# Kernel tuning notes

Hardware: AMD Instinct MI355X
Metric: run time of the kernel (lower is better)

The kernel has to match this reference:

```python
import jax, jax.numpy as jnp
import numpy as np

# GraphConvolutionSparse forward:
#   x = sparse_dropout(X)            (dropout=0.0 -> identity, kept faithful)
#   h = X @ W                        (sparse-dense matmul via segment_sum)
#   h = A @ h                        (sparse-dense matmul via segment_sum)
#   out = relu(h)

DROPOUT = 0.0  # layer default; keep_prob = 1 - dropout

def setup_inputs() -> dict:
    key = jax.random.key(0)
    k1, k2, k3, k4, k5, k6, k7 = jax.random.split(key, 7)
    N = 100000       # nodes
    D_IN = 512       # input feature dim
    D_OUT = 128      # output feature dim
    NNZ_X = 800000   # nonzeros in sparse feature matrix
    N_E = 1600000    # adjacency nonzeros (edges)
    x_vals = jax.random.normal(k1, (NNZ_X,), dtype=jnp.float32)
    x_rows = jax.random.randint(k2, (NNZ_X,), 0, N, dtype=jnp.int32)
    x_cols = jax.random.randint(k3, (NNZ_X,), 0, D_IN, dtype=jnp.int32)
    adj_vals = jax.random.uniform(k4, (N_E,), dtype=jnp.float32)
    adj_rows = jax.random.randint(k5, (N_E,), 0, N, dtype=jnp.int32)
    adj_cols = jax.random.randint(k6, (N_E,), 0, N, dtype=jnp.int32)
    init_range = np.sqrt(6.0 / (D_IN + D_OUT)).astype(np.float32)
    W = jax.random.uniform(k7, (D_IN, D_OUT), minval=-init_range, maxval=init_range, dtype=jnp.float32)
    return {"x_vals": x_vals, "x_rows": x_rows, "x_cols": x_cols,
            "adj_vals": adj_vals, "adj_rows": adj_rows, "adj_cols": adj_cols,
            "W": W, "n_nodes": N}

def reference(x_vals, x_rows, x_cols, adj_vals, adj_rows, adj_cols, W, n_nodes):
    keep_prob = 1.0 - DROPOUT
    # sparse dropout: with dropout=0.0 the mask keeps all entries and scale is 1,
    # so it reduces to the deterministic identity (faithful to tf semantics).
    vals = x_vals * (1.0 / keep_prob)
    # h = X @ W : gather weight rows by feature column, scale, scatter-add by node row
    xw = jax.ops.segment_sum(vals[:, None] * W[x_cols], x_rows, num_segments=n_nodes)  # [N, D_OUT]
    # out = A @ h : gather source-node rows, scale by edge weight, scatter-add to dest
    agg = jax.ops.segment_sum(adj_vals[:, None] * xw[adj_cols], adj_rows, num_segments=n_nodes)  # [N, D_OUT]
    return jax.nn.relu(agg)
```

## Files before the change

kernel.cpp:

```cpp
#include <hip/hip_runtime.h>
#include <hip/hip_fp16.h>


#define DOUT 128
#define RB 64
#define RB_BITS 6
#define NBMAX 2048
#define CAPL 2048
#define COLMASK 131071
#define CTH 256
#define CWAVES 4
#define CAPX 768
#define CAPA 1408

static inline size_t align_up(size_t x, size_t a) { return (x + a - 1) & ~(a - 1); }

__device__ inline int wave_incl_scan(int v, int lane) {
    #pragma unroll
    for (int off = 1; off < 64; off <<= 1) {
        int up = __shfl_up(v, off, 64);
        if (lane >= off) v += up;
    }
    return v;
}

__global__ __launch_bounds__(256) void wh_precompute(const float* __restrict__ W,
                                                     __half2* __restrict__ Wh, int total) {
    int i = blockIdx.x * 256 + threadIdx.x;
    if (i < total) {
        int c = i >> 6, l = i & 63;
        Wh[i] = __floats2half2_rn(W[(c << 7) + 2 * l], W[(c << 7) + 2 * l + 1]);
    }
}

__global__ __launch_bounds__(256) void hist_coarse(const int* __restrict__ xr, int nx,
                                                   const int* __restrict__ ar, int na,
                                                   int* __restrict__ cx, int* __restrict__ ca) {
    __shared__ int h[2 * NBMAX];
    for (int i = threadIdx.x; i < 2 * NBMAX; i += 256) h[i] = 0;
    __syncthreads();
    int base = blockIdx.x * 4096;
    int tot = nx + na;
    #pragma unroll
    for (int k = 0; k < 16; ++k) {
        int i = base + k * 256 + threadIdx.x;
        if (i < tot) {
            if (i < nx) atomicAdd(&h[xr[i] >> RB_BITS], 1);
            else        atomicAdd(&h[NBMAX + (ar[i - nx] >> RB_BITS)], 1);
        }
    }
    __syncthreads();
    for (int i = threadIdx.x; i < 2 * NBMAX; i += 256) {
        int c = h[i];
        if (c) {
            if (i < NBMAX) atomicAdd(&cx[i], c);
            else           atomicAdd(&ca[i - NBMAX], c);
        }
    }
}

__global__ __launch_bounds__(1024) void scan_nb(const int* __restrict__ cx, const int* __restrict__ ca,
                                                int* __restrict__ bx, int* __restrict__ ba,
                                                int* __restrict__ curx, int* __restrict__ cura, int nb) {
    const int* c = blockIdx.x ? ca : cx;
    int* bs  = blockIdx.x ? ba : bx;
    int* cur = blockIdx.x ? cura : curx;
    __shared__ int wsum[16];
    __shared__ int woff[16];
    __shared__ int carry_s, chunk_tot;
    int tid = threadIdx.x, lane = tid & 63, wid = tid >> 6;
    if (tid == 0) carry_s = 0;
    __syncthreads();
    for (int base = 0; base < nb; base += 1024) {
        int i = base + tid;
        int v = (i < nb) ? c[i] : 0;
        int incl = wave_incl_scan(v, lane);
        if (lane == 63) wsum[wid] = incl;
        __syncthreads();
        if (wid == 0 && lane < 16) {
            int s = wsum[lane];
            int is = s;
            #pragma unroll
            for (int off = 1; off < 16; off <<= 1) {
                int up = __shfl_up(is, off, 64);
                if (lane >= off) is += up;
            }
            woff[lane] = is - s;
            if (lane == 15) chunk_tot = is;
        }
        __syncthreads();
        int excl = incl - v + woff[wid] + carry_s;
        if (i < nb) { bs[i] = excl; cur[i] = excl; }
        __syncthreads();
        if (tid == 0) carry_s += chunk_tot;
        __syncthreads();
    }
    if (tid == 0) bs[nb] = carry_s;
}

__global__ __launch_bounds__(512) void bucket_scatter2(const int* __restrict__ xr, const int* __restrict__ xc,
                                                       const float* __restrict__ xv, int nx,
                                                       const int* __restrict__ ar, const int* __restrict__ ac,
                                                       const float* __restrict__ av, int na,
                                                       int* __restrict__ curx, int* __restrict__ cura,
                                                       int2* __restrict__ stx, int2* __restrict__ sta,
                                                       int nb, int nblk_x, int capx, int capa) {
    const int* rows; const int* cols; const float* vals; int n; int* gcur; int2* stage; int base; int cap;
    if (blockIdx.x < nblk_x) {
        rows = xr; cols = xc; vals = xv; n = nx; gcur = curx; stage = stx;
        base = blockIdx.x * 4096; cap = capx;
    } else {
        rows = ar; cols = ac; vals = av; n = na; gcur = cura; stage = sta;
        base = (blockIdx.x - nblk_x) * 4096; cap = capa;
    }
    __shared__ int h[NBMAX];
    __shared__ int bcur[NBMAX];
    for (int i = threadIdx.x; i < nb; i += 512) h[i] = 0;
    __syncthreads();
    int rr[8]; int cc[8]; float vv[8];
    #pragma unroll
    for (int k = 0; k < 8; ++k) {
        int i = base + k * 512 + threadIdx.x;
        rr[k] = -1;
        if (i < n) {
            rr[k] = rows[i]; cc[k] = cols[i]; vv[k] = vals[i];
            atomicAdd(&h[rr[k] >> RB_BITS], 1);
        }
    }
    __syncthreads();
    for (int b = threadIdx.x; b < nb; b += 512) {
        int c = h[b];
        if (c) {
            int r = atomicAdd(&gcur[b], c);
            bcur[b] = (cap > 0) ? (b * cap + r) : r;
        }
    }
    __syncthreads();
    #pragma unroll
    for (int k = 0; k < 8; ++k) {
        if (rr[k] >= 0) {
            int b = rr[k] >> RB_BITS;
            int p = atomicAdd(&bcur[b], 1);
            if (cap == 0 || p < b * cap + cap)
                stage[p] = make_int2(((rr[k] & (RB - 1)) << 17) | cc[k], __float_as_int(vv[k]));
        }
    }
}

__global__ __launch_bounds__(CTH) void consumer_xw(const int* __restrict__ bx, const int* __restrict__ gcnt,
                                                   const int2* __restrict__ stage,
                                                   const __half2* __restrict__ Wh, __half2* __restrict__ xwh,
                                                   int N, int cap) {
    __shared__ int2 sp[CAPL];
    __shared__ int hoff[RB + 1];
    __shared__ int curs[RB];
    int b = blockIdx.x;
    int s, cnt;
    if (cap > 0) { s = b * cap; cnt = min(gcnt[b], cap); }
    else         { s = bx[b]; cnt = bx[b + 1] - s; }
    int tid = threadIdx.x, lane = tid & 63, wid = tid >> 6;
    bool fast = (cnt <= CAPL);
    if (tid < RB) curs[tid] = 0;
    __syncthreads();
    if (fast) {
        for (int i = tid; i < cnt; i += CTH)
            atomicAdd(&curs[(stage[s + i].x >> 17) & (RB - 1)], 1);
    }
    __syncthreads();
    if (wid == 0) {
        int v = curs[lane];
        int incl = wave_incl_scan(v, lane);
        int excl = incl - v;
        hoff[lane] = excl;
        curs[lane] = excl;
        if (lane == 63) hoff[RB] = incl;
    }
    __syncthreads();
    if (fast) {
        for (int i = tid; i < cnt; i += CTH) {
            int2 p = stage[s + i];
            int r = (p.x >> 17) & (RB - 1);
            sp[atomicAdd(&curs[r], 1)] = p;
        }
    }
    __syncthreads();
    int row0 = b << RB_BITS;
    #pragma unroll 1
    for (int rr = 0; rr < RB / CWAVES; ++rr) {
        int r = wid + rr * CWAVES;
        int grow = row0 + r;
        if (grow >= N) continue;
        float ax = 0.f, ay = 0.f;
        if (fast) {
            int j = hoff[r], o1 = hoff[r + 1];
            for (; j + 3 < o1; j += 4) {
                int2 c0 = sp[j], c1 = sp[j + 1], c2 = sp[j + 2], c3 = sp[j + 3];
                float2 w0 = __half22float2(Wh[((size_t)(c0.x & COLMASK) << 6) + lane]);
                float2 w1 = __half22float2(Wh[((size_t)(c1.x & COLMASK) << 6) + lane]);
                float2 w2 = __half22float2(Wh[((size_t)(c2.x & COLMASK) << 6) + lane]);
                float2 w3 = __half22float2(Wh[((size_t)(c3.x & COLMASK) << 6) + lane]);
                float v0 = __int_as_float(c0.y), v1 = __int_as_float(c1.y);
                float v2 = __int_as_float(c2.y), v3 = __int_as_float(c3.y);
                ax += v0 * w0.x + v1 * w1.x + v2 * w2.x + v3 * w3.x;
                ay += v0 * w0.y + v1 * w1.y + v2 * w2.y + v3 * w3.y;
            }
            for (; j < o1; ++j) {
                int2 c0 = sp[j];
                float2 w0 = __half22float2(Wh[((size_t)(c0.x & COLMASK) << 6) + lane]);
                float v0 = __int_as_float(c0.y);
                ax += v0 * w0.x; ay += v0 * w0.y;
            }
        } else {
            for (int j = 0; j < cnt; ++j) {
                int2 c0 = stage[s + j];
                if (((c0.x >> 17) & (RB - 1)) == r) {
                    float2 w0 = __half22float2(Wh[((size_t)(c0.x & COLMASK) << 6) + lane]);
                    float v0 = __int_as_float(c0.y);
                    ax += v0 * w0.x; ay += v0 * w0.y;
                }
            }
        }
        xwh[((size_t)grow << 6) + lane] = __float22half2_rn(make_float2(ax, ay));
    }
}

__global__ __launch_bounds__(CTH) void consumer_adj(const int* __restrict__ ba, const int* __restrict__ gcnt,
                                                    const int2* __restrict__ stage,
                                                    const __half2* __restrict__ xwh, float* __restrict__ out,
                                                    int N, int cap) {
    __shared__ int2 sp[CAPL];
    __shared__ int hoff[RB + 1];
    __shared__ int curs[RB];
    int b = blockIdx.x;
    int s, cnt;
    if (cap > 0) { s = b * cap; cnt = min(gcnt[b], cap); }
    else         { s = ba[b]; cnt = ba[b + 1] - s; }
    int tid = threadIdx.x, lane = tid & 63, wid = tid >> 6;
    bool fast = (cnt <= CAPL);
    if (tid < RB) curs[tid] = 0;
    __syncthreads();
    if (fast) {
        for (int i = tid; i < cnt; i += CTH)
            atomicAdd(&curs[(stage[s + i].x >> 17) & (RB - 1)], 1);
    }
    __syncthreads();
    if (wid == 0) {
        int v = curs[lane];
        int incl = wave_incl_scan(v, lane);
        int excl = incl - v;
        hoff[lane] = excl;
        curs[lane] = excl;
        if (lane == 63) hoff[RB] = incl;
    }
    __syncthreads();
    if (fast) {
        for (int i = tid; i < cnt; i += CTH) {
            int2 p = stage[s + i];
            int r = (p.x >> 17) & (RB - 1);
            sp[atomicAdd(&curs[r], 1)] = p;
        }
    }
    __syncthreads();
    int row0 = b << RB_BITS;
    #pragma unroll 1
    for (int rr = 0; rr < RB / CWAVES; ++rr) {
        int r = wid + rr * CWAVES;
        int grow = row0 + r;
        if (grow >= N) continue;
        float ax = 0.f, ay = 0.f;
        if (fast) {
            int j = hoff[r], o1 = hoff[r + 1];
            for (; j + 3 < o1; j += 4) {
                int2 c0 = sp[j], c1 = sp[j + 1], c2 = sp[j + 2], c3 = sp[j + 3];
                float2 h0 = __half22float2(xwh[((size_t)(c0.x & COLMASK) << 6) + lane]);
                float2 h1 = __half22float2(xwh[((size_t)(c1.x & COLMASK) << 6) + lane]);
                float2 h2 = __half22float2(xwh[((size_t)(c2.x & COLMASK) << 6) + lane]);
                float2 h3 = __half22float2(xwh[((size_t)(c3.x & COLMASK) << 6) + lane]);
                float v0 = __int_as_float(c0.y), v1 = __int_as_float(c1.y);
                float v2 = __int_as_float(c2.y), v3 = __int_as_float(c3.y);
                ax += v0 * h0.x + v1 * h1.x + v2 * h2.x + v3 * h3.x;
                ay += v0 * h0.y + v1 * h1.y + v2 * h2.y + v3 * h3.y;
            }
            for (; j < o1; ++j) {
                int2 c0 = sp[j];
                float2 h0 = __half22float2(xwh[((size_t)(c0.x & COLMASK) << 6) + lane]);
                float v0 = __int_as_float(c0.y);
                ax += v0 * h0.x; ay += v0 * h0.y;
            }
        } else {
            for (int j = 0; j < cnt; ++j) {
                int2 c0 = stage[s + j];
                if (((c0.x >> 17) & (RB - 1)) == r) {
                    float2 h0 = __half22float2(xwh[((size_t)(c0.x & COLMASK) << 6) + lane]);
                    float v0 = __int_as_float(c0.y);
                    ax += v0 * h0.x; ay += v0 * h0.y;
                }
            }
        }
        ((float2*)(out + (size_t)grow * DOUT))[lane] = make_float2(fmaxf(ax, 0.f), fmaxf(ay, 0.f));
    }
}

__global__ void spmm_xw_atomic(const float* __restrict__ x_vals, const int* __restrict__ x_rows,
                               const int* __restrict__ x_cols, const float* __restrict__ W,
                               float* __restrict__ xw, int nnz) {
    long long t = (long long)blockIdx.x * blockDim.x + threadIdx.x;
    int i = (int)(t >> 7), d = (int)(t & 127);
    if (i >= nnz) return;
    atomicAdd(&xw[(long long)x_rows[i] * DOUT + d], x_vals[i] * W[(long long)x_cols[i] * DOUT + d]);
}
__global__ void spmm_adj_atomic(const float* __restrict__ adj_vals, const int* __restrict__ adj_rows,
                                const int* __restrict__ adj_cols, const float* __restrict__ xw,
                                float* __restrict__ out, int n_e) {
    long long t = (long long)blockIdx.x * blockDim.x + threadIdx.x;
    int e = (int)(t >> 7), d = (int)(t & 127);
    if (e >= n_e) return;
    atomicAdd(&out[(long long)adj_rows[e] * DOUT + d], adj_vals[e] * xw[(long long)adj_cols[e] * DOUT + d]);
}
__global__ void relu_kernel(float4* __restrict__ out, int n4) {
    int i = blockIdx.x * blockDim.x + threadIdx.x;
    if (i >= n4) return;
    float4 v = out[i];
    v.x = fmaxf(v.x, 0.f); v.y = fmaxf(v.y, 0.f);
    v.z = fmaxf(v.z, 0.f); v.w = fmaxf(v.w, 0.f);
    out[i] = v;
}

extern "C" void kernel_launch(void* const* d_in, const int* in_sizes, int n_in,
                              void* d_out, int out_size, void* d_ws, size_t ws_size,
                              hipStream_t stream) {
    const float* x_vals   = (const float*)d_in[0];
    const int*   x_rows   = (const int*)d_in[1];
    const int*   x_cols   = (const int*)d_in[2];
    const float* adj_vals = (const float*)d_in[3];
    const int*   adj_rows = (const int*)d_in[4];
    const int*   adj_cols = (const int*)d_in[5];
    const float* W        = (const float*)d_in[6];
    float* out = (float*)d_out;

    const int nnz_x = in_sizes[0];
    const int n_e   = in_sizes[3];
    const int N     = out_size / DOUT;
    const int D_IN  = in_sizes[6] / DOUT;
    const int nb    = (N + RB - 1) / RB;

    char* ws = (char*)d_ws;
    size_t off = 0;
    size_t xw_off   = off; off = align_up(off + (size_t)N * DOUT * sizeof(__half), 128);
    size_t wh_off   = off; off = align_up(off + (size_t)D_IN * 64 * sizeof(__half2), 128);
    size_t cx_off   = off; off += (size_t)NBMAX * sizeof(int);
    size_t ca_off   = off; off = align_up(off + (size_t)NBMAX * sizeof(int), 128);
    size_t bx_off   = off; off = align_up(off + (size_t)(NBMAX + 1) * sizeof(int), 128);
    size_t baoff    = off; off = align_up(off + (size_t)(NBMAX + 1) * sizeof(int), 128);
    size_t curx_off = off; off = align_up(off + (size_t)NBMAX * sizeof(int), 128);
    size_t cura_off = off; off = align_up(off + (size_t)NBMAX * sizeof(int), 128);
    size_t head = off;
    size_t sxc_off = head;
    size_t sac_off = align_up(sxc_off + (size_t)nb * CAPX * sizeof(int2), 128);
    size_t needed_cap = align_up(sac_off + (size_t)nb * CAPA * sizeof(int2), 128);
    size_t sxm_off = head;
    size_t sam_off = align_up(sxm_off + (size_t)nnz_x * sizeof(int2), 128);
    size_t needed_mid = align_up(sam_off + (size_t)n_e * sizeof(int2), 128);

    bool ok_dims = (nb <= NBMAX) && (N <= (COLMASK + 1));

    if (ok_dims && ws_size >= needed_cap) {
        __half2* xwh  = (__half2*)(ws + xw_off);
        __half2* Wh   = (__half2*)(ws + wh_off);
        int*  cx      = (int*)(ws + cx_off);
        int*  ca      = (int*)(ws + ca_off);
        int2* stage_x = (int2*)(ws + sxc_off);
        int2* stage_a = (int2*)(ws + sac_off);

        hipMemsetAsync(cx, 0, 2 * (size_t)NBMAX * sizeof(int), stream);
        int whtot = D_IN * 64;
        wh_precompute<<<(whtot + 255) / 256, 256, 0, stream>>>(W, Wh, whtot);

        int nblk_x = (nnz_x + 4095) / 4096;
        int nblk_a = (n_e + 4095) / 4096;
        bucket_scatter2<<<nblk_x + nblk_a, 512, 0, stream>>>(x_rows, x_cols, x_vals, nnz_x,
                                                             adj_rows, adj_cols, adj_vals, n_e,
                                                             cx, ca, stage_x, stage_a, nb, nblk_x,
                                                             CAPX, CAPA);
        consumer_xw<<<nb, CTH, 0, stream>>>(nullptr, cx, stage_x, Wh, xwh, N, CAPX);
        consumer_adj<<<nb, CTH, 0, stream>>>(nullptr, ca, stage_a, xwh, out, N, CAPA);
    } else if (ok_dims && ws_size >= needed_mid) {
        __half2* xwh  = (__half2*)(ws + xw_off);
        __half2* Wh   = (__half2*)(ws + wh_off);
        int*  cx      = (int*)(ws + cx_off);
        int*  ca      = (int*)(ws + ca_off);
        int*  bx      = (int*)(ws + bx_off);
        int*  ba      = (int*)(ws + baoff);
        int*  curx    = (int*)(ws + curx_off);
        int*  cura    = (int*)(ws + cura_off);
        int2* stage_x = (int2*)(ws + sxm_off);
        int2* stage_a = (int2*)(ws + sam_off);

        hipMemsetAsync(cx, 0, 2 * (size_t)NBMAX * sizeof(int), stream);
        int whtot = D_IN * 64;
        wh_precompute<<<(whtot + 255) / 256, 256, 0, stream>>>(W, Wh, whtot);

        int tot = nnz_x + n_e;
        hist_coarse<<<(tot + 4095) / 4096, 256, 0, stream>>>(x_rows, nnz_x, adj_rows, n_e, cx, ca);
        scan_nb<<<2, 1024, 0, stream>>>(cx, ca, bx, ba, curx, cura, nb);

        int nblk_x = (nnz_x + 4095) / 4096;
        int nblk_a = (n_e + 4095) / 4096;
        bucket_scatter2<<<nblk_x + nblk_a, 512, 0, stream>>>(x_rows, x_cols, x_vals, nnz_x,
                                                             adj_rows, adj_cols, adj_vals, n_e,
                                                             curx, cura, stage_x, stage_a, nb, nblk_x,
                                                             0, 0);
        consumer_xw<<<nb, CTH, 0, stream>>>(bx, nullptr, stage_x, Wh, xwh, N, 0);
        consumer_adj<<<nb, CTH, 0, stream>>>(ba, nullptr, stage_a, xwh, out, N, 0);
    } else {
        float* xw = (float*)ws;
        hipMemsetAsync(xw, 0, (size_t)out_size * sizeof(float), stream);
        hipMemsetAsync(out, 0, (size_t)out_size * sizeof(float), stream);
        long long t1 = (long long)nnz_x * DOUT;
        spmm_xw_atomic<<<(int)((t1 + 255) / 256), 256, 0, stream>>>(x_vals, x_rows, x_cols, W, xw, nnz_x);
        long long t2 = (long long)n_e * DOUT;
        spmm_adj_atomic<<<(int)((t2 + 255) / 256), 256, 0, stream>>>(adj_vals, adj_rows, adj_cols, xw, out, n_e);
        relu_kernel<<<(out_size / 4 + 255) / 256, 256, 0, stream>>>((float4*)out, out_size / 4);
    }
}
```

Before: 218.3 us.

## Use per-row counts from scatter and vectorized 16-lane-group gathers in consumers

The scatter kernel now also counts entries per row with global atomics, so both consumers can build row offsets directly instead of re-histogramming the staged entries in shared memory. The consumer inner loops are restructured so each group of 16 lanes handles one nonzero with 16-byte loads of a full 128-wide half row, four nonzeros per wave step, then reduces the partial sums across groups with shuffles. The separate memset is folded into a combined prep kernel that also converts W to half. This trades extra global atomics in the scatter for fewer shared-memory passes and wider, more parallel gathers. If a bucket overflows its capacity while the row total still fits the local buffer, the consumers can read uninitialised shared slots.

```diff
diff --git a/kernel.cpp b/kernel.cpp
--- a/kernel.cpp
+++ b/kernel.cpp
@@ -24,10 +24,12 @@
     return v;
 }
 
-__global__ __launch_bounds__(256) void wh_precompute(const float* __restrict__ W,
-                                                     __half2* __restrict__ Wh, int total) {
+__global__ __launch_bounds__(256) void prep_kernel(int* __restrict__ cnts, int ncnt,
+                                                   const float* __restrict__ W,
+                                                   __half2* __restrict__ Wh, int whtot) {
     int i = blockIdx.x * 256 + threadIdx.x;
-    if (i < total) {
+    if (i < ncnt) cnts[i] = 0;
+    if (i < whtot) {
         int c = i >> 6, l = i & 63;
         Wh[i] = __floats2half2_rn(W[(c << 7) + 2 * l], W[(c << 7) + 2 * l + 1]);
     }
@@ -103,14 +105,16 @@
                                                        const int* __restrict__ ar, const int* __restrict__ ac,
                                                        const float* __restrict__ av, int na,
                                                        int* __restrict__ curx, int* __restrict__ cura,
+                                                       int* __restrict__ crx, int* __restrict__ cra,
                                                        int2* __restrict__ stx, int2* __restrict__ sta,
                                                        int nb, int nblk_x, int capx, int capa) {
-    const int* rows; const int* cols; const float* vals; int n; int* gcur; int2* stage; int base; int cap;
+    const int* rows; const int* cols; const float* vals; int n;
+    int* gcur; int* cnt_row; int2* stage; int base; int cap;
     if (blockIdx.x < nblk_x) {
-        rows = xr; cols = xc; vals = xv; n = nx; gcur = curx; stage = stx;
+        rows = xr; cols = xc; vals = xv; n = nx; gcur = curx; cnt_row = crx; stage = stx;
         base = blockIdx.x * 4096; cap = capx;
     } else {
-        rows = ar; cols = ac; vals = av; n = na; gcur = cura; stage = sta;
+        rows = ar; cols = ac; vals = av; n = na; gcur = cura; cnt_row = cra; stage = sta;
         base = (blockIdx.x - nblk_x) * 4096; cap = capa;
     }
     __shared__ int h[NBMAX];
@@ -125,6 +129,7 @@
         if (i < n) {
             rr[k] = rows[i]; cc[k] = cols[i]; vv[k] = vals[i];
             atomicAdd(&h[rr[k] >> RB_BITS], 1);
+            atomicAdd(&cnt_row[rr[k]], 1);
         }
     }
     __syncthreads();
@@ -147,7 +152,9 @@
     }
 }
 
+
 __global__ __launch_bounds__(CTH) void consumer_xw(const int* __restrict__ bx, const int* __restrict__ gcnt,
+                                                   const int* __restrict__ cnt_row,
                                                    const int2* __restrict__ stage,
                                                    const __half2* __restrict__ Wh, __half2* __restrict__ xwh,
                                                    int N, int cap) {
@@ -159,13 +166,8 @@
     if (cap > 0) { s = b * cap; cnt = min(gcnt[b], cap); }
     else         { s = bx[b]; cnt = bx[b + 1] - s; }
     int tid = threadIdx.x, lane = tid & 63, wid = tid >> 6;
-    bool fast = (cnt <= CAPL);
-    if (tid < RB) curs[tid] = 0;
-    __syncthreads();
-    if (fast) {
-        for (int i = tid; i < cnt; i += CTH)
-            atomicAdd(&curs[(stage[s + i].x >> 17) & (RB - 1)], 1);
-    }
+    int row0 = b << RB_BITS;
+    if (tid < RB) curs[tid] = (row0 + tid < N) ? cnt_row[row0 + tid] : 0;
     __syncthreads();
     if (wid == 0) {
         int v = curs[lane];
@@ -176,6 +178,7 @@
         if (lane == 63) hoff[RB] = incl;
     }
     __syncthreads();
+    bool fast = (hoff[RB] <= CAPL);
     if (fast) {
         for (int i = tid; i < cnt; i += CTH) {
             int2 p = stage[s + i];
@@ -184,33 +187,47 @@
         }
     }
     __syncthreads();
-    int row0 = b << RB_BITS;
+    int grp = lane >> 4, ss = lane & 15;
     #pragma unroll 1
     for (int rr = 0; rr < RB / CWAVES; ++rr) {
         int r = wid + rr * CWAVES;
         int grow = row0 + r;
         if (grow >= N) continue;
-        float ax = 0.f, ay = 0.f;
         if (fast) {
-            int j = hoff[r], o1 = hoff[r + 1];
-            for (; j + 3 < o1; j += 4) {
-                int2 c0 = sp[j], c1 = sp[j + 1], c2 = sp[j + 2], c3 = sp[j + 3];
-                float2 w0 = __half22float2(Wh[((size_t)(c0.x & COLMASK) << 6) + lane]);
-                float2 w1 = __half22float2(Wh[((size_t)(c1.x & COLMASK) << 6) + lane]);
-                float2 w2 = __half22float2(Wh[((size_t)(c2.x & COLMASK) << 6) + lane]);
-                float2 w3 = __half22float2(Wh[((size_t)(c3.x & COLMASK) << 6) + lane]);
-                float v0 = __int_as_float(c0.y), v1 = __int_as_float(c1.y);
-                float v2 = __int_as_float(c2.y), v3 = __int_as_float(c3.y);
-                ax += v0 * w0.x + v1 * w1.x + v2 * w2.x + v3 * w3.x;
-                ay += v0 * w0.y + v1 * w1.y + v2 * w2.y + v3 * w3.y;
-            }
-            for (; j < o1; ++j) {
-                int2 c0 = sp[j];
-                float2 w0 = __half22float2(Wh[((size_t)(c0.x & COLMASK) << 6) + lane]);
-                float v0 = __int_as_float(c0.y);
-                ax += v0 * w0.x; ay += v0 * w0.y;
+            int j0 = hoff[r], j1 = hoff[r + 1];
+            float a0 = 0.f, a1 = 0.f, a2 = 0.f, a3 = 0.f, a4 = 0.f, a5 = 0.f, a6 = 0.f, a7 = 0.f;
+            #pragma unroll 2
+            for (int j = j0; j < j1; j += 4) {
+                int idx = j + grp;
+                bool valid = idx < j1;
+                int2 c = sp[valid ? idx : j0];
+                float v = valid ? __int_as_float(c.y) : 0.f;
+                float4 w = ((const float4*)(Wh + ((size_t)(c.x & COLMASK) << 6)))[ss];
+                float2 p0 = __half22float2(*(const __half2*)&w.x);
+                float2 p1 = __half22float2(*(const __half2*)&w.y);
+                float2 p2 = __half22float2(*(const __half2*)&w.z);
+                float2 p3 = __half22float2(*(const __half2*)&w.w);
+                a0 += v * p0.x; a1 += v * p0.y; a2 += v * p1.x; a3 += v * p1.y;
+                a4 += v * p2.x; a5 += v * p2.y; a6 += v * p3.x; a7 += v * p3.y;
+            }
+            a0 += __shfl_xor(a0, 16); a1 += __shfl_xor(a1, 16);
+            a2 += __shfl_xor(a2, 16); a3 += __shfl_xor(a3, 16);
+            a4 += __shfl_xor(a4, 16); a5 += __shfl_xor(a5, 16);
+            a6 += __shfl_xor(a6, 16); a7 += __shfl_xor(a7, 16);
+            a0 += __shfl_xor(a0, 32); a1 += __shfl_xor(a1, 32);
+            a2 += __shfl_xor(a2, 32); a3 += __shfl_xor(a3, 32);
+            a4 += __shfl_xor(a4, 32); a5 += __shfl_xor(a5, 32);
+            a6 += __shfl_xor(a6, 32); a7 += __shfl_xor(a7, 32);
+            if (grp == 0) {
+                __half2 h0 = __floats2half2_rn(a0, a1);
+                __half2 h1 = __floats2half2_rn(a2, a3);
+                __half2 h2 = __floats2half2_rn(a4, a5);
+                __half2 h3 = __floats2half2_rn(a6, a7);
+                int4 pk = make_int4(*(int*)&h0, *(int*)&h1, *(int*)&h2, *(int*)&h3);
+                ((int4*)(xwh + ((size_t)grow << 6)))[ss] = pk;
             }
         } else {
+            float ax = 0.f, ay = 0.f;
             for (int j = 0; j < cnt; ++j) {
                 int2 c0 = stage[s + j];
                 if (((c0.x >> 17) & (RB - 1)) == r) {
@@ -219,12 +236,13 @@
                     ax += v0 * w0.x; ay += v0 * w0.y;
                 }
             }
-        }
-        xwh[((size_t)grow << 6) + lane] = __float22half2_rn(make_float2(ax, ay));
+            xwh[((size_t)grow << 6) + lane] = __float22half2_rn(make_float2(ax, ay));
+        }
     }
 }
 
 __global__ __launch_bounds__(CTH) void consumer_adj(const int* __restrict__ ba, const int* __restrict__ gcnt,
+                                                    const int* __restrict__ cnt_row,
                                                     const int2* __restrict__ stage,
                                                     const __half2* __restrict__ xwh, float* __restrict__ out,
                                                     int N, int cap) {
@@ -236,13 +254,8 @@
     if (cap > 0) { s = b * cap; cnt = min(gcnt[b], cap); }
     else         { s = ba[b]; cnt = ba[b + 1] - s; }
     int tid = threadIdx.x, lane = tid & 63, wid = tid >> 6;
-    bool fast = (cnt <= CAPL);
-    if (tid < RB) curs[tid] = 0;
-    __syncthreads();
-    if (fast) {
-        for (int i = tid; i < cnt; i += CTH)
-            atomicAdd(&curs[(stage[s + i].x >> 17) & (RB - 1)], 1);
-    }
+    int row0 = b << RB_BITS;
+    if (tid < RB) curs[tid] = (row0 + tid < N) ? cnt_row[row0 + tid] : 0;
     __syncthreads();
     if (wid == 0) {
         int v = curs[lane];
@@ -253,6 +266,7 @@
         if (lane == 63) hoff[RB] = incl;
     }
     __syncthreads();
+    bool fast = (hoff[RB] <= CAPL);
     if (fast) {
         for (int i = tid; i < cnt; i += CTH) {
             int2 p = stage[s + i];
@@ -261,33 +275,44 @@
         }
     }
     __syncthreads();
-    int row0 = b << RB_BITS;
+    int grp = lane >> 4, ss = lane & 15;
     #pragma unroll 1
     for (int rr = 0; rr < RB / CWAVES; ++rr) {
         int r = wid + rr * CWAVES;
         int grow = row0 + r;
         if (grow >= N) continue;
-        float ax = 0.f, ay = 0.f;
         if (fast) {
-            int j = hoff[r], o1 = hoff[r + 1];
-            for (; j + 3 < o1; j += 4) {
-                int2 c0 = sp[j], c1 = sp[j + 1], c2 = sp[j + 2], c3 = sp[j + 3];
-                float2 h0 = __half22float2(xwh[((size_t)(c0.x & COLMASK) << 6) + lane]);
-                float2 h1 = __half22float2(xwh[((size_t)(c1.x & COLMASK) << 6) + lane]);
-                float2 h2 = __half22float2(xwh[((size_t)(c2.x & COLMASK) << 6) + lane]);
-                float2 h3 = __half22float2(xwh[((size_t)(c3.x & COLMASK) << 6) + lane]);
-                float v0 = __int_as_float(c0.y), v1 = __int_as_float(c1.y);
-                float v2 = __int_as_float(c2.y), v3 = __int_as_float(c3.y);
-                ax += v0 * h0.x + v1 * h1.x + v2 * h2.x + v3 * h3.x;
-                ay += v0 * h0.y + v1 * h1.y + v2 * h2.y + v3 * h3.y;
-            }
-            for (; j < o1; ++j) {
-                int2 c0 = sp[j];
-                float2 h0 = __half22float2(xwh[((size_t)(c0.x & COLMASK) << 6) + lane]);
-                float v0 = __int_as_float(c0.y);
-                ax += v0 * h0.x; ay += v0 * h0.y;
+            int j0 = hoff[r], j1 = hoff[r + 1];
+            float a0 = 0.f, a1 = 0.f, a2 = 0.f, a3 = 0.f, a4 = 0.f, a5 = 0.f, a6 = 0.f, a7 = 0.f;
+            #pragma unroll 2
+            for (int j = j0; j < j1; j += 4) {
+                int idx = j + grp;
+                bool valid = idx < j1;
+                int2 c = sp[valid ? idx : j0];
+                float v = valid ? __int_as_float(c.y) : 0.f;
+                float4 w = ((const float4*)(xwh + ((size_t)(c.x & COLMASK) << 6)))[ss];
+                float2 p0 = __half22float2(*(const __half2*)&w.x);
+                float2 p1 = __half22float2(*(const __half2*)&w.y);
+                float2 p2 = __half22float2(*(const __half2*)&w.z);
+                float2 p3 = __half22float2(*(const __half2*)&w.w);
+                a0 += v * p0.x; a1 += v * p0.y; a2 += v * p1.x; a3 += v * p1.y;
+                a4 += v * p2.x; a5 += v * p2.y; a6 += v * p3.x; a7 += v * p3.y;
+            }
+            a0 += __shfl_xor(a0, 16); a1 += __shfl_xor(a1, 16);
+            a2 += __shfl_xor(a2, 16); a3 += __shfl_xor(a3, 16);
+            a4 += __shfl_xor(a4, 16); a5 += __shfl_xor(a5, 16);
+            a6 += __shfl_xor(a6, 16); a7 += __shfl_xor(a7, 16);
+            a0 += __shfl_xor(a0, 32); a1 += __shfl_xor(a1, 32);
+            a2 += __shfl_xor(a2, 32); a3 += __shfl_xor(a3, 32);
+            a4 += __shfl_xor(a4, 32); a5 += __shfl_xor(a5, 32);
+            a6 += __shfl_xor(a6, 32); a7 += __shfl_xor(a7, 32);
+            if (grp == 0) {
+                float4* dst = (float4*)(out + (size_t)grow * DOUT);
+                dst[2 * ss]     = make_float4(fmaxf(a0, 0.f), fmaxf(a1, 0.f), fmaxf(a2, 0.f), fmaxf(a3, 0.f));
+                dst[2 * ss + 1] = make_float4(fmaxf(a4, 0.f), fmaxf(a5, 0.f), fmaxf(a6, 0.f), fmaxf(a7, 0.f));
             }
         } else {
+            float ax = 0.f, ay = 0.f;
             for (int j = 0; j < cnt; ++j) {
                 int2 c0 = stage[s + j];
                 if (((c0.x >> 17) & (RB - 1)) == r) {
@@ -296,8 +321,8 @@
                     ax += v0 * h0.x; ay += v0 * h0.y;
                 }
             }
-        }
-        ((float2*)(out + (size_t)grow * DOUT))[lane] = make_float2(fmaxf(ax, 0.f), fmaxf(ay, 0.f));
+            ((float2*)(out + (size_t)grow * DOUT))[lane] = make_float2(fmaxf(ax, 0.f), fmaxf(ay, 0.f));
+        }
     }
 }
 
@@ -349,11 +374,11 @@
     size_t xw_off   = off; off = align_up(off + (size_t)N * DOUT * sizeof(__half), 128);
     size_t wh_off   = off; off = align_up(off + (size_t)D_IN * 64 * sizeof(__half2), 128);
     size_t cx_off   = off; off += (size_t)NBMAX * sizeof(int);
-    size_t ca_off   = off; off = align_up(off + (size_t)NBMAX * sizeof(int), 128);
+    size_t ca_off   = off; off += (size_t)NBMAX * sizeof(int);
+    size_t crx_off  = off; off += (size_t)N * sizeof(int);
+    size_t cra_off  = off; off = align_up(off + (size_t)N * sizeof(int), 128);
     size_t bx_off   = off; off = align_up(off + (size_t)(NBMAX + 1) * sizeof(int), 128);
     size_t baoff    = off; off = align_up(off + (size_t)(NBMAX + 1) * sizeof(int), 128);
-    size_t curx_off = off; off = align_up(off + (size_t)NBMAX * sizeof(int), 128);
-    size_t cura_off = off; off = align_up(off + (size_t)NBMAX * sizeof(int), 128);
     size_t head = off;
     size_t sxc_off = head;
     size_t sac_off = align_up(sxc_off + (size_t)nb * CAPX * sizeof(int2), 128);
@@ -363,55 +388,56 @@
     size_t needed_mid = align_up(sam_off + (size_t)n_e * sizeof(int2), 128);
 
     bool ok_dims = (nb <= NBMAX) && (N <= (COLMASK + 1));
+    const int ncnt = 2 * NBMAX + 2 * N;
+    const int whtot = D_IN * 64;
+    const int prep_n = (ncnt > whtot ? ncnt : whtot);
 
     if (ok_dims && ws_size >= needed_cap) {
         __half2* xwh  = (__half2*)(ws + xw_off);
         __half2* Wh   = (__half2*)(ws + wh_off);
         int*  cx      = (int*)(ws + cx_off);
         int*  ca      = (int*)(ws + ca_off);
+        int*  crx     = (int*)(ws + crx_off);
+        int*  cra     = (int*)(ws + cra_off);
         int2* stage_x = (int2*)(ws + sxc_off);
         int2* stage_a = (int2*)(ws + sac_off);
 
-        hipMemsetAsync(cx, 0, 2 * (size_t)NBMAX * sizeof(int), stream);
-        int whtot = D_IN * 64;
-        wh_precompute<<<(whtot + 255) / 256, 256, 0, stream>>>(W, Wh, whtot);
+        prep_kernel<<<(prep_n + 255) / 256, 256, 0, stream>>>(cx, ncnt, W, Wh, whtot);
 
         int nblk_x = (nnz_x + 4095) / 4096;
         int nblk_a = (n_e + 4095) / 4096;
         bucket_scatter2<<<nblk_x + nblk_a, 512, 0, stream>>>(x_rows, x_cols, x_vals, nnz_x,
                                                              adj_rows, adj_cols, adj_vals, n_e,
-                                                             cx, ca, stage_x, stage_a, nb, nblk_x,
-                                                             CAPX, CAPA);
-        consumer_xw<<<nb, CTH, 0, stream>>>(nullptr, cx, stage_x, Wh, xwh, N, CAPX);
-        consumer_adj<<<nb, CTH, 0, stream>>>(nullptr, ca, stage_a, xwh, out, N, CAPA);
+                                                             cx, ca, crx, cra, stage_x, stage_a,
+                                                             nb, nblk_x, CAPX, CAPA);
+        consumer_xw<<<nb, CTH, 0, stream>>>(nullptr, cx, crx, stage_x, Wh, xwh, N, CAPX);
+        consumer_adj<<<nb, CTH, 0, stream>>>(nullptr, ca, cra, stage_a, xwh, out, N, CAPA);
     } else if (ok_dims && ws_size >= needed_mid) {
         __half2* xwh  = (__half2*)(ws + xw_off);
         __half2* Wh   = (__half2*)(ws + wh_off);
         int*  cx      = (int*)(ws + cx_off);
         int*  ca      = (int*)(ws + ca_off);
+        int*  crx     = (int*)(ws + crx_off);
+        int*  cra     = (int*)(ws + cra_off);
         int*  bx      = (int*)(ws + bx_off);
         int*  ba      = (int*)(ws + baoff);
-        int*  curx    = (int*)(ws + curx_off);
-        int*  cura    = (int*)(ws + cura_off);
         int2* stage_x = (int2*)(ws + sxm_off);
         int2* stage_a = (int2*)(ws + sam_off);
 
-        hipMemsetAsync(cx, 0, 2 * (size_t)NBMAX * sizeof(int), stream);
-        int whtot = D_IN * 64;
-        wh_precompute<<<(whtot + 255) / 256, 256, 0, stream>>>(W, Wh, whtot);
+        prep_kernel<<<(prep_n + 255) / 256, 256, 0, stream>>>(cx, ncnt, W, Wh, whtot);
 
         int tot = nnz_x + n_e;
         hist_coarse<<<(tot + 4095) / 4096, 256, 0, stream>>>(x_rows, nnz_x, adj_rows, n_e, cx, ca);
-        scan_nb<<<2, 1024, 0, stream>>>(cx, ca, bx, ba, curx, cura, nb);
+        scan_nb<<<2, 1024, 0, stream>>>(cx, ca, bx, ba, cx, ca, nb);
 
         int nblk_x = (nnz_x + 4095) / 4096;
         int nblk_a = (n_e + 4095) / 4096;
         bucket_scatter2<<<nblk_x + nblk_a, 512, 0, stream>>>(x_rows, x_cols, x_vals, nnz_x,
                                                              adj_rows, adj_cols, adj_vals, n_e,
-                                                             curx, cura, stage_x, stage_a, nb, nblk_x,
-                                                             0, 0);
-        consumer_xw<<<nb, CTH, 0, stream>>>(bx, nullptr, stage_x, Wh, xwh, N, 0);
-        consumer_adj<<<nb, CTH, 0, stream>>>(ba, nullptr, stage_a, xwh, out, N, 0);
+                                                             cx, ca, crx, cra, stage_x, stage_a,
+                                                             nb, nblk_x, 0, 0);
+        consumer_xw<<<nb, CTH, 0, stream>>>(bx, nullptr, crx, stage_x, Wh, xwh, N, 0);
+        consumer_adj<<<nb, CTH, 0, stream>>>(ba, nullptr, cra, stage_a, xwh, out, N, 0);
     } else {
         float* xw = (float*)ws;
         hipMemsetAsync(xw, 0, (size_t)out_size * sizeof(float), stream);
```

After: 305.4 us. +39.9%, slower.
